# Optimization experiments

Hardware: AMD Instinct MI355X
Metric: run time of the kernel (lower is better)

The kernel has to match this reference:

```python
import jax, jax.numpy as jnp
import numpy as np

K = 512          # codebook size
D = 128          # embedding dim (== num_hiddens, required by the module wiring)
COMMIT = 0.25    # commitment cost
EPS = 1e-10


def conv2d(x, w, b):
    # x: [B,C,H,W], w: [O,I,3,3] (torch OIHW), stride 1, pad 1 -> same spatial size
    y = jax.lax.conv_general_dilated(
        x, w, window_strides=(1, 1), padding=((1, 1), (1, 1)),
        dimension_numbers=("NCHW", "OIHW", "NCHW"))
    return y + b[None, :, None, None]


def conv_transpose2d(x, w, b):
    # torch ConvTranspose2d weight layout is [I, O, kH, kW]; with stride=1, pad=1, k=3
    # it equals a regular conv with the kernel spatially flipped and in/out swapped.
    w2 = jnp.flip(w, axis=(-2, -1)).transpose(1, 0, 2, 3)  # -> OIHW
    return conv2d(x, w2, b)


def setup_inputs() -> dict:
    key = jax.random.key(0)
    ks = jax.random.split(key, 12)
    s = 0.05  # keep activations well-scaled through 8 stacked convs
    return {
        "x":       jax.random.normal(ks[0], (16, 3, 128, 128), jnp.float32),
        "enc_w0":  jax.random.normal(ks[1], (128, 3, 3, 3), jnp.float32) * s,
        "enc_b0":  jax.random.normal(ks[2], (128,), jnp.float32) * s,
        "enc_wh":  jax.random.normal(ks[3], (3, 128, 128, 3, 3), jnp.float32) * s,
        "enc_bh":  jax.random.normal(ks[4], (3, 128), jnp.float32) * s,
        "pre_w":   jax.random.normal(ks[5], (128, 128), jnp.float32) * s,
        "pre_b":   jax.random.normal(ks[6], (128,), jnp.float32) * s,
        "codebook": jax.random.normal(ks[7], (K, D), jnp.float32),  # EMA init: normal_()
        "dec_wh":  jax.random.normal(ks[8], (3, 128, 128, 3, 3), jnp.float32) * s,
        "dec_bh":  jax.random.normal(ks[9], (3, 128), jnp.float32) * s,
        "dec_wl":  jax.random.normal(ks[10], (128, 3, 3, 3), jnp.float32) * s,
        "dec_bl":  jax.random.normal(ks[11], (3,), jnp.float32) * s,
    }


def reference(x, enc_w0, enc_b0, enc_wh, enc_bh, pre_w, pre_b, codebook,
              dec_wh, dec_bh, dec_wl, dec_bl):
    # ---- encoder: stack of 3x3 stride-1 convs (no nonlinearity in the source) ----
    z = conv2d(x, enc_w0, enc_b0)
    for i in range(enc_wh.shape[0]):
        z = conv2d(z, enc_wh[i], enc_bh[i])
    # pre-VQ 1x1 conv
    z = jnp.einsum("bchw,oc->bohw", z, pre_w) + pre_b[None, :, None, None]

    # ---- VectorQuantizerEMA forward (eval mode: EMA buffers not updated) ----
    zt = jnp.transpose(z, (0, 2, 3, 1))          # [B,H,W,D]
    B, H, W, _ = zt.shape
    flat = zt.reshape(-1, D)                      # [N,D]
    d = (jnp.sum(flat * flat, axis=1, keepdims=True)
         + jnp.sum(codebook * codebook, axis=1)
         - 2.0 * flat @ codebook.T)               # [N,K]
    idx = jnp.argmin(d, axis=1)                   # [N]
    quantized = codebook[idx].reshape(B, H, W, D) # gather == one-hot @ codebook

    # commitment loss (EMA variant: only e_latent term)
    e_latent = jnp.mean((jax.lax.stop_gradient(quantized) - zt) ** 2)
    loss = COMMIT * e_latent

    # straight-through estimator
    quantized = zt + jax.lax.stop_gradient(quantized - zt)

    # perplexity from empirical code usage
    counts = jax.ops.segment_sum(jnp.ones_like(idx, jnp.float32), idx, num_segments=K)
    avg_probs = counts / flat.shape[0]
    perplexity = jnp.exp(-jnp.sum(avg_probs * jnp.log(avg_probs + EPS)))

    q = jnp.transpose(quantized, (0, 3, 1, 2))    # back to NCHW

    # ---- decoder: stack of 3x3 stride-1 conv-transposes ----
    h = q
    for i in range(dec_wh.shape[0]):
        h = conv_transpose2d(h, dec_wh[i], dec_bh[i])
    x_recon = conv_transpose2d(h, dec_wl, dec_bl)

    return loss, x_recon, perplexity
```

## Files before the change

### kernel.cpp

```cpp
#include <hip/hip_runtime.h>

namespace {

constexpr int NB = 16, HH = 128, WW = 128, KK = 512, DD = 128;
constexpr int NPIX = NB * HH * WW;
constexpr int NELEM = NPIX * DD;
constexpr int XRECON = NB * 3 * HH * WW;
constexpr int VQ_BLK_PX = 64;
constexpr int VQ_BLOCKS = NPIX / VQ_BLK_PX;

using bf16x8 = __attribute__((ext_vector_type(8))) short;
using f32x4 = __attribute__((ext_vector_type(4))) float;

__device__ __forceinline__ ushort f2bf(float f) {
  unsigned u = __float_as_uint(f);
  return (ushort)((u + 0x7FFFu + ((u >> 16) & 1u)) >> 16);
}

__global__ void zero_counts(int* __restrict__ counts) {
  const int t = threadIdx.x;
  counts[t] = 0;
  counts[t + 256] = 0;
}

__device__ __forceinline__ int swz(int px) { return px + ((px >> 5) << 2); }

__global__ void repack_w(const float* __restrict__ w, float* __restrict__ wr) {
  int i = blockIdx.x * 256 + threadIdx.x;
  int oc = i & 127;
  int tap = (i >> 7) % 9;
  int ci = i / (9 * 128);
  wr[i] = w[(oc * 128 + ci) * 9 + tap];
}

__global__ void repack_wb16(const float* __restrict__ w, ushort* __restrict__ wr) {
  int i = blockIdx.x * 256 + threadIdx.x;
  int j = i & 7;
  int oc = (i >> 3) & 127;
  int cib = (i >> 10) & 15;
  int tap = i >> 14;
  int ci = cib * 8 + j;
  int ky = tap / 3, kx = tap % 3;
  float v = w[((size_t)ci * 128 + oc) * 9 + (2 - ky) * 3 + (2 - kx)];
  wr[i] = f2bf(v);
}

template <int CT>
__global__ __launch_bounds__(256, 5) void conv3x3_s(
    const float* __restrict__ in, const float* __restrict__ wr,
    const float* __restrict__ bias, float* __restrict__ out) {
  __shared__ __align__(16) float s_in[CT][3][148];
  const int tid = threadIdx.x;
  const int b = blockIdx.x >> 7;
  const int y = blockIdx.x & 127;
  const int lane = tid & 63;
  const int wv = __builtin_amdgcn_readfirstlane(tid >> 6);
  const int oc0 = wv << 5;
  const int px0 = lane << 1;

  float acc[32][2];
#pragma unroll
  for (int k = 0; k < 32; ++k) { acc[k][0] = 0.f; acc[k][1] = 0.f; }

  const int f_lo = swz(px0);
  const int f_hi = swz(px0 + 2);

#pragma unroll 1
  for (int ci0 = 0; ci0 < 128; ci0 += CT) {
    for (int i = tid; i < CT * 390; i += 256) {
      int ci = i / 390;
      int rem = i - ci * 390;
      int r = rem / 130;
      int px = rem - r * 130;
      int yy = y + r - 1;
      int xx = px - 1;
      float v = 0.f;
      if (yy >= 0 && yy < HH && xx >= 0 && xx < WW)
        v = in[((b * 128 + ci0 + ci) * HH + yy) * WW + xx];
      s_in[ci][r][swz(px)] = v;
    }
    __syncthreads();
#pragma unroll 1
    for (int ci = 0; ci < CT; ++ci) {
      float ind[3][4];
#pragma unroll
      for (int r = 0; r < 3; ++r) {
        float2 a = *reinterpret_cast<const float2*>(&s_in[ci][r][f_lo]);
        float2 c = *reinterpret_cast<const float2*>(&s_in[ci][r][f_hi]);
        ind[r][0] = a.x; ind[r][1] = a.y; ind[r][2] = c.x; ind[r][3] = c.y;
      }
      const float* wp = wr + (size_t)(ci0 + ci) * 9 * 128 + oc0;
#pragma unroll
      for (int r = 0; r < 3; ++r) {
#pragma unroll
        for (int dx = 0; dx < 3; ++dx) {
          const float* wt = wp + (r * 3 + dx) * 128;
          float ws[32];
#pragma unroll
          for (int k = 0; k < 32; ++k) ws[k] = wt[k];
          float v0 = ind[r][dx], v1 = ind[r][dx + 1];
#pragma unroll
          for (int k = 0; k < 32; ++k) {
            acc[k][0] = __fmaf_rn(ws[k], v0, acc[k][0]);
            acc[k][1] = __fmaf_rn(ws[k], v1, acc[k][1]);
          }
        }
      }
    }
    __syncthreads();
  }
#pragma unroll
  for (int k = 0; k < 32; ++k) {
    int oc = oc0 + k;
    float bv = bias[oc];
    float2 v = {acc[k][0] + bv, acc[k][1] + bv};
    *reinterpret_cast<float2*>(out + ((b * 128 + oc) * HH + y) * WW + px0) = v;
  }
}

__global__ __launch_bounds__(256, 3) void conv_l1(
    const float* __restrict__ in, const float* __restrict__ w,
    const float* __restrict__ bias, float* __restrict__ out) {
  __shared__ __align__(16) double s_in[3][3][74];
  __shared__ __align__(16) float s_w[27][132];
  const int tid = threadIdx.x;
  const int b = blockIdx.x >> 8;
  const int y = (blockIdx.x >> 1) & 127;
  const int x0base = (blockIdx.x & 1) << 6;
  const int ocg = tid >> 3;
  const int pxg = tid & 7;
  const int x0 = pxg * 8;
  const int f0 = pxg * 9;

  double acc[4][8];
#pragma unroll
  for (int k = 0; k < 4; ++k)
#pragma unroll
    for (int p = 0; p < 8; ++p) acc[k][p] = 0.0;

  for (int i = tid; i < 3 * 198; i += 256) {
    int ci = i / 198;
    int rem = i - ci * 198;
    int r = rem / 66;
    int px = rem - r * 66;
    int yy = y + r - 1;
    int xx = x0base + px - 1;
    float v = 0.f;
    if (yy >= 0 && yy < HH && xx >= 0 && xx < WW)
      v = in[((b * 3 + ci) * HH + yy) * WW + xx];
    s_in[ci][r][px + (px >> 3)] = (double)v;
  }
  for (int i = tid; i < 128 * 27; i += 256) {
    int oc = i / 27;
    int j = i - oc * 27;
    s_w[j][oc] = w[oc * 27 + j];
  }
  __syncthreads();
#pragma unroll 1
  for (int ci = 0; ci < 3; ++ci) {
#pragma unroll
    for (int r = 0; r < 3; ++r) {
      double ind[10];
#pragma unroll
      for (int m = 0; m < 8; ++m) ind[m] = s_in[ci][r][f0 + m];
      ind[8] = s_in[ci][r][f0 + 9];
      ind[9] = s_in[ci][r][f0 + 10];
#pragma unroll
      for (int dx = 0; dx < 3; ++dx) {
        float4 w4 = *reinterpret_cast<const float4*>(&s_w[ci * 9 + r * 3 + dx][ocg * 4]);
        double wd[4] = {(double)w4.x, (double)w4.y, (double)w4.z, (double)w4.w};
#pragma unroll
        for (int k = 0; k < 4; ++k)
#pragma unroll
          for (int p = 0; p < 8; ++p) acc[k][p] += wd[k] * ind[p + dx];
      }
    }
  }
#pragma unroll
  for (int k = 0; k < 4; ++k) {
    int oc = ocg * 4 + k;
    double bv = (double)bias[oc];
    float* op = out + ((b * 128 + oc) * HH + y) * WW + x0base + x0;
    float4 v = {(float)(acc[k][0] + bv), (float)(acc[k][1] + bv),
                (float)(acc[k][2] + bv), (float)(acc[k][3] + bv)};
    float4 v2 = {(float)(acc[k][4] + bv), (float)(acc[k][5] + bv),
                 (float)(acc[k][6] + bv), (float)(acc[k][7] + bv)};
    *reinterpret_cast<float4*>(op) = v;
    *reinterpret_cast<float4*>(op + 4) = v2;
  }
}

__global__ __launch_bounds__(256, 3) void prevq_nhwc(
    const float* __restrict__ in, const float* __restrict__ wmat,
    const float* __restrict__ bias, float* __restrict__ flat) {
  __shared__ __align__(16) float s_z[32][68];
  __shared__ __align__(16) float s_w[32][132];
  const int tid = threadIdx.x;
  const int b = blockIdx.x >> 8;
  const int y = (blockIdx.x >> 1) & 127;
  const int x0base = (blockIdx.x & 1) << 6;
  const int ocg = tid >> 3;
  const int pxg = tid & 7;
  float acc[4][8];
#pragma unroll
  for (int k = 0; k < 4; ++k)
#pragma unroll
    for (int p = 0; p < 8; ++p) acc[k][p] = 0.f;

#pragma unroll 1
  for (int c0 = 0; c0 < 128; c0 += 32) {
    for (int t = tid; t < 32 * 64; t += 256) {
      int c = t >> 6, px = t & 63;
      s_z[c][px] = in[((b * 128 + c0 + c) * HH + y) * WW + x0base + px];
    }
    for (int t = tid; t < 32 * 128; t += 256) {
      int o = t >> 5, c = t & 31;
      s_w[c][o] = wmat[o * 128 + c0 + c];
    }
    __syncthreads();
#pragma unroll 1
    for (int c = 0; c < 32; ++c) {
      float f8[8];
#pragma unroll
      for (int p = 0; p < 8; ++p) f8[p] = s_z[c][pxg * 8 + p];
      float4 w4 = *reinterpret_cast<const float4*>(&s_w[c][ocg * 4]);
      float wd[4] = {w4.x, w4.y, w4.z, w4.w};
#pragma unroll
      for (int k = 0; k < 4; ++k)
#pragma unroll
        for (int p = 0; p < 8; ++p) acc[k][p] = __fmaf_rn(wd[k], f8[p], acc[k][p]);
    }
    __syncthreads();
  }
  float bv[4];
#pragma unroll
  for (int k = 0; k < 4; ++k) bv[k] = bias[ocg * 4 + k];
  const int pixbase = (b * HH + y) * WW + x0base + pxg * 8;
#pragma unroll
  for (int p = 0; p < 8; ++p) {
    float* op = flat + (pixbase + p) * DD + ocg * 4;
#pragma unroll
    for (int k = 0; k < 4; ++k) op[k] = __fadd_rn(acc[k][p], bv[k]);
  }
}

__device__ __forceinline__ float pairwise8_sq(const float* v) {
  float r[8];
#pragma unroll
  for (int j = 0; j < 8; ++j) r[j] = __fmul_rn(v[j], v[j]);
#pragma unroll
  for (int i = 8; i < 128; i += 8)
#pragma unroll
    for (int j = 0; j < 8; ++j) r[j] = __fadd_rn(r[j], __fmul_rn(v[i + j], v[i + j]));
  return __fadd_rn(__fadd_rn(__fadd_rn(r[0], r[1]), __fadd_rn(r[2], r[3])),
                   __fadd_rn(__fadd_rn(r[4], r[5]), __fadd_rn(r[6], r[7])));
}

constexpr int SF_OFF = 0;
constexpr int SC_OFF = 33792;
constexpr int SRB_OFF = SC_OFF;
constexpr int SRI_OFF = SC_OFF + 4352;
constexpr int SCN_OFF = SC_OFF + 33792;
constexpr int SZN_OFF = SCN_OFF + 256;
constexpr int SIDX_OFF = SZN_OFF + 256;
constexpr int SRED_OFF = SIDX_OFF + 256;
constexpr int SMEM_BYTES = SRED_OFF + 32;

__global__ __launch_bounds__(256, 2) void vq_fused(
    const float* __restrict__ flat, const float* __restrict__ codebook,
    ushort* __restrict__ q16, float* __restrict__ partial, int* __restrict__ counts) {
  __shared__ __align__(16) char smem[SMEM_BYTES];
  float (*s_f)[132] = reinterpret_cast<float (*)[132]>(smem + SF_OFF);
  float (*s_c)[132] = reinterpret_cast<float (*)[132]>(smem + SC_OFF);
  float (*s_rb)[4][17] = reinterpret_cast<float (*)[4][17]>(smem + SRB_OFF);
  int (*s_ri)[4][17] = reinterpret_cast<int (*)[4][17]>(smem + SRI_OFF);
  float* s_cn = reinterpret_cast<float*>(smem + SCN_OFF);
  float* s_zn = reinterpret_cast<float*>(smem + SZN_OFF);
  int* s_idx = reinterpret_cast<int*>(smem + SIDX_OFF);
  double* s_red = reinterpret_cast<double*>(smem + SRED_OFF);

  const int tid = threadIdx.x;
  const int n0 = blockIdx.x * VQ_BLK_PX;
  const int pxg = tid & 15;
  const int cg = tid >> 4;

  for (int t = tid; t < VQ_BLK_PX * 128; t += 256) {
    int i = t >> 7, d = t & 127;
    s_f[i][d] = flat[(n0 + i) * DD + d];
  }
  __syncthreads();
  if (tid < VQ_BLK_PX) s_zn[tid] = pairwise8_sq(&s_f[tid][0]);

  float best[4] = {3.402823466e+38f, 3.402823466e+38f,
                   3.402823466e+38f, 3.402823466e+38f};
  int bi[4] = {0, 0, 0, 0};

#pragma unroll 1
  for (int c0 = 0; c0 < KK; c0 += 64) {
    for (int t = tid; t < 64 * 128; t += 256) {
      int cc = t >> 7, d = t & 127;
      s_c[cc][d] = codebook[(c0 + cc) * DD + d];
    }
    __syncthreads();
    if (tid < 64) s_cn[tid] = pairwise8_sq(&s_c[tid][0]);
    __syncthreads();
    float acc[4][4];
#pragma unroll
    for (int i = 0; i < 4; ++i)
#pragma unroll
      for (int j = 0; j < 4; ++j) acc[i][j] = 0.f;
#pragma unroll 1
    for (int d0 = 0; d0 < 128; d0 += 4) {
      float4 f4[4], c4[4];
#pragma unroll
      for (int i = 0; i < 4; ++i)
        f4[i] = *reinterpret_cast<const float4*>(&s_f[pxg * 4 + i][d0]);
#pragma unroll
      for (int j = 0; j < 4; ++j)
        c4[j] = *reinterpret_cast<const float4*>(&s_c[cg * 4 + j][d0]);
#pragma unroll
      for (int i = 0; i < 4; ++i) {
#pragma unroll
        for (int j = 0; j < 4; ++j) {
          acc[i][j] = __fmaf_rn(f4[i].x, c4[j].x, acc[i][j]);
          acc[i][j] = __fmaf_rn(f4[i].y, c4[j].y, acc[i][j]);
          acc[i][j] = __fmaf_rn(f4[i].z, c4[j].z, acc[i][j]);
          acc[i][j] = __fmaf_rn(f4[i].w, c4[j].w, acc[i][j]);
        }
      }
    }
#pragma unroll
    for (int i = 0; i < 4; ++i)
#pragma unroll
      for (int j = 0; j < 4; ++j) {
        float score = __fsub_rn(__fadd_rn(s_zn[pxg * 4 + i], s_cn[cg * 4 + j]),
                                __fmul_rn(2.0f, acc[i][j]));
        int code = c0 + cg * 4 + j;
        if (score < best[i]) { best[i] = score; bi[i] = code; }
      }
    __syncthreads();
  }
#pragma unroll
  for (int i = 0; i < 4; ++i) {
    s_rb[pxg][i][cg] = best[i];
    s_ri[pxg][i][cg] = bi[i];
  }
  __syncthreads();
  if (tid < 16) {
    for (int i = 0; i < 4; ++i) {
      float m = s_rb[tid][i][0];
      int mi = s_ri[tid][i][0];
      for (int g = 1; g < 16; ++g) {
        float v = s_rb[tid][i][g];
        int vi = s_ri[tid][i][g];
        if (v < m || (v == m && vi < mi)) { m = v; mi = vi; }
      }
      s_idx[tid * 4 + i] = mi;
    }
  }
  __syncthreads();
  if (tid < VQ_BLK_PX) atomicAdd(&counts[s_idx[tid]], 1);

  const int px = tid & 63;
  const int dg = tid >> 6;
  const int n = n0 + px;
  const int k = s_idx[px];
  const float* crow = codebook + k * DD + dg * 32;
  ushort* qb = q16 + (size_t)n * 128 + dg * 32;
  double s = 0.0;
#pragma unroll 4
  for (int j = 0; j < 32; ++j) {
    float e = crow[j];
    double dd = (double)e - (double)s_f[px][dg * 32 + j];
    s += dd * dd;
    qb[j] = f2bf(e);
  }
  for (int off = 32; off; off >>= 1) s += __shfl_down(s, off);
  if ((tid & 63) == 0) s_red[tid >> 6] = s;
  __syncthreads();
  if (tid == 0)
    partial[blockIdx.x] = (float)(s_red[0] + s_red[1] + s_red[2] + s_red[3]);
}

template <bool LAST>
__global__ __launch_bounds__(256, 4) void dec_mfma(
    const ushort* __restrict__ inq, const ushort* __restrict__ wb,
    const float* __restrict__ bias, float* __restrict__ outf,
    ushort* __restrict__ outq) {
  const int b = blockIdx.x >> 7;
  const int y = blockIdx.x & 127;
  const int lane = threadIdx.x & 63;
  const int wv = threadIdx.x >> 6;
  const int oc0 = wv << 5;
  const int lrow = lane & 15;
  const int lk = lane >> 4;

  f32x4 acc[8][2];
#pragma unroll
  for (int mt = 0; mt < 8; ++mt)
#pragma unroll
    for (int nt = 0; nt < 2; ++nt) acc[mt][nt] = (f32x4){0.f, 0.f, 0.f, 0.f};

#pragma unroll 1
  for (int tap = 0; tap < 9; ++tap) {
    const int ky = tap / 3, kx = tap % 3;
    const int yy = y + ky - 1;
    const bool yok = (yy >= 0) && (yy < HH);
    const ushort* wtap = wb + tap * (16 * 128 * 8);
    const ushort* rowp = inq + ((size_t)(b * HH + yy) * WW) * 128;
#pragma unroll 1
    for (int cb = 0; cb < 4; ++cb) {
      const int cib = cb * 4 + lk;
      bf16x8 bfr0 = *reinterpret_cast<const bf16x8*>(wtap + ((size_t)(cib * 128) + oc0 + lrow) * 8);
      bf16x8 bfr1 = *reinterpret_cast<const bf16x8*>(wtap + ((size_t)(cib * 128) + oc0 + 16 + lrow) * 8);
#pragma unroll
      for (int mt = 0; mt < 8; ++mt) {
        const int xx = mt * 16 + lrow + kx - 1;
        bf16x8 af = {0, 0, 0, 0, 0, 0, 0, 0};
        if (yok && xx >= 0 && xx < WW)
          af = *reinterpret_cast<const bf16x8*>(rowp + (size_t)xx * 128 + cib * 8);
        acc[mt][0] = __builtin_amdgcn_mfma_f32_16x16x32_bf16(af, bfr0, acc[mt][0], 0, 0, 0);
        acc[mt][1] = __builtin_amdgcn_mfma_f32_16x16x32_bf16(af, bfr1, acc[mt][1], 0, 0, 0);
      }
    }
  }
#pragma unroll
  for (int nt = 0; nt < 2; ++nt) {
    const int oc = oc0 + nt * 16 + lrow;
    const float bv = bias[oc];
    if constexpr (LAST) {
#pragma unroll
      for (int mt = 0; mt < 8; ++mt) {
        const int px = mt * 16 + lk * 4;
        float4 v = {acc[mt][nt][0] + bv, acc[mt][nt][1] + bv,
                    acc[mt][nt][2] + bv, acc[mt][nt][3] + bv};
        *reinterpret_cast<float4*>(outf + ((size_t)(b * 128 + oc) * HH + y) * WW + px) = v;
      }
    } else {
#pragma unroll
      for (int mt = 0; mt < 8; ++mt) {
#pragma unroll
        for (int m = 0; m < 4; ++m) {
          const int px = mt * 16 + lk * 4 + m;
          outq[((size_t)(b * HH + y) * WW + px) * 128 + oc] = f2bf(acc[mt][nt][m] + bv);
        }
      }
    }
  }
}

__global__ __launch_bounds__(256, 3) void conv_out3(
    const float* __restrict__ in, const float* __restrict__ w,
    const float* __restrict__ bias, float* __restrict__ out) {
  __shared__ float s_in[16][4][130];
  __shared__ float s_w[128][28];
  const int tid = threadIdx.x;
  const int b = blockIdx.x >> 6;
  const int y0 = (blockIdx.x & 63) << 1;
  const int yloc = tid >> 7;
  const int x = tid & 127;
  const int y = y0 + yloc;
  for (int i = tid; i < 128 * 27; i += 256) {
    int ci = i / 27, rem = i % 27, oc = rem / 9, tap = rem % 9;
    int ky = tap / 3, kx = tap % 3;
    s_w[ci][tap * 3 + oc] = w[((ci * 3 + oc) * 3 + (2 - ky)) * 3 + (2 - kx)];
  }
  float acc[3] = {0.f, 0.f, 0.f};
#pragma unroll 1
  for (int ci0 = 0; ci0 < 128; ci0 += 16) {
    for (int i = tid; i < 16 * 520; i += 256) {
      int ci = i / 520;
      int rem = i - ci * 520;
      int r = rem / 130;
      int px = rem - r * 130;
      int yy = y0 + r - 1;
      float v = 0.f;
      if (yy >= 0 && yy < HH && px >= 1 && px <= 128)
        v = in[((b * 128 + ci0 + ci) * HH + yy) * WW + (px - 1)];
      s_in[ci][r][px] = v;
    }
    __syncthreads();
#pragma unroll 1
    for (int ci = 0; ci < 16; ++ci) {
#pragma unroll
      for (int r = 0; r < 3; ++r) {
        float i3[3] = {s_in[ci][yloc + r][x], s_in[ci][yloc + r][x + 1],
                       s_in[ci][yloc + r][x + 2]};
#pragma unroll
        for (int dx = 0; dx < 3; ++dx)
#pragma unroll
          for (int oc = 0; oc < 3; ++oc)
            acc[oc] += s_w[ci0 + ci][(r * 3 + dx) * 3 + oc] * i3[dx];
      }
    }
    __syncthreads();
  }
#pragma unroll
  for (int oc = 0; oc < 3; ++oc)
    out[((b * 3 + oc) * HH + y) * WW + x] = acc[oc] + bias[oc];
}

__global__ void finalize(const float* __restrict__ partial,
                         const int* __restrict__ counts, float* __restrict__ out) {
  __shared__ double redh[4], reds[4];
  const int tid = threadIdx.x;
  double h = 0.0;
  for (int k = tid; k < KK; k += 256) {
    double p = (double)counts[k] * (1.0 / (double)NPIX);
    h += p * log(p + 1e-10);
  }
  double s = 0.0;
  for (int i = tid; i < VQ_BLOCKS; i += 256) s += (double)partial[i];
  for (int off = 32; off; off >>= 1) {
    h += __shfl_down(h, off);
    s += __shfl_down(s, off);
  }
  if ((tid & 63) == 0) { redh[tid >> 6] = h; reds[tid >> 6] = s; }
  __syncthreads();
  if (tid == 0) {
    double Hs = redh[0] + redh[1] + redh[2] + redh[3];
    double Ss = reds[0] + reds[1] + reds[2] + reds[3];
    out[0] = (float)(0.25 * Ss * (1.0 / (double)NELEM));
    out[1 + XRECON] = (float)exp(-Hs);
  }
}

}

extern "C" void kernel_launch(void* const* d_in, const int* in_sizes, int n_in,
                              void* d_out, int out_size, void* d_ws, size_t ws_size,
                              hipStream_t stream) {
  (void)in_sizes; (void)n_in; (void)out_size; (void)ws_size;
  const float* x       = (const float*)d_in[0];
  const float* enc_w0  = (const float*)d_in[1];
  const float* enc_b0  = (const float*)d_in[2];
  const float* enc_wh  = (const float*)d_in[3];
  const float* enc_bh  = (const float*)d_in[4];
  const float* pre_w   = (const float*)d_in[5];
  const float* pre_b   = (const float*)d_in[6];
  const float* codebook= (const float*)d_in[7];
  const float* dec_wh  = (const float*)d_in[8];
  const float* dec_bh  = (const float*)d_in[9];
  const float* dec_wl  = (const float*)d_in[10];
  const float* dec_bl  = (const float*)d_in[11];
  float* out = (float*)d_out;

  float* A = (float*)d_ws;
  float* Bf = A + NELEM;
  ushort* Q0 = (ushort*)Bf;
  ushort* Q1 = Q0 + NELEM;

  int* counts = (int*)(out + 1);
  float* partial = out + 1 + KK;
  float* wbuf = out + 4612;
  ushort* wb0 = (ushort*)(wbuf + 147456);
  ushort* wb1 = wb0 + 147456;
  ushort* wb2 = wb1 + 147456;

  const int LSTRIDE = 128 * 128 * 9;
  const int RGRID = NB * HH;
  const int CGRID = NB * HH * 2;
  const int WGRID = 576;

  zero_counts<<<1, 256, 0, stream>>>(counts);

  conv_l1<<<CGRID, 256, 0, stream>>>(x, enc_w0, enc_b0, A);
  repack_w<<<WGRID, 256, 0, stream>>>(enc_wh, wbuf);
  conv3x3_s<16><<<RGRID, 256, 0, stream>>>(A, wbuf, enc_bh, Bf);
  repack_w<<<WGRID, 256, 0, stream>>>(enc_wh + LSTRIDE, wbuf);
  conv3x3_s<16><<<RGRID, 256, 0, stream>>>(Bf, wbuf, enc_bh + 128, A);
  repack_w<<<WGRID, 256, 0, stream>>>(enc_wh + 2 * LSTRIDE, wbuf);
  conv3x3_s<16><<<RGRID, 256, 0, stream>>>(A, wbuf, enc_bh + 256, Bf);

  prevq_nhwc<<<CGRID, 256, 0, stream>>>(Bf, pre_w, pre_b, A);

  repack_wb16<<<WGRID, 256, 0, stream>>>(dec_wh, wb0);
  repack_wb16<<<WGRID, 256, 0, stream>>>(dec_wh + LSTRIDE, wb1);
  repack_wb16<<<WGRID, 256, 0, stream>>>(dec_wh + 2 * LSTRIDE, wb2);

  vq_fused<<<VQ_BLOCKS, 256, 0, stream>>>(A, codebook, Q0, partial, counts);

  finalize<<<1, 256, 0, stream>>>(partial, counts, out);

  dec_mfma<false><<<RGRID, 256, 0, stream>>>(Q0, wb0, dec_bh, nullptr, Q1);
  dec_mfma<false><<<RGRID, 256, 0, stream>>>(Q1, wb1, dec_bh + 128, nullptr, Q0);
  dec_mfma<true><<<RGRID, 256, 0, stream>>>(Q0, wb2, dec_bh + 256, A, nullptr);
  conv_out3<<<NB * HH / 2, 256, 0, stream>>>(A, dec_wl, dec_bl, out + 1);
}
```

Baseline: 4.738 ms.

## Retile encoder 3x3 conv to two rows per block with split output channels

```diff
diff --git a/kernel.cpp b/kernel.cpp
--- a/kernel.cpp
+++ b/kernel.cpp
@@ -46,33 +46,36 @@
 }
 
 template <int CT>
-__global__ __launch_bounds__(256, 5) void conv3x3_s(
+__global__ __launch_bounds__(256, 4) void conv3x3_s2(
     const float* __restrict__ in, const float* __restrict__ wr,
     const float* __restrict__ bias, float* __restrict__ out) {
-  __shared__ __align__(16) float s_in[CT][3][148];
+  __shared__ __align__(16) float s_in[CT][4][148];
   const int tid = threadIdx.x;
+  const int ocb = blockIdx.x & 1;
+  const int y0 = ((blockIdx.x >> 1) & 63) << 1;
   const int b = blockIdx.x >> 7;
-  const int y = blockIdx.x & 127;
   const int lane = tid & 63;
   const int wv = __builtin_amdgcn_readfirstlane(tid >> 6);
-  const int oc0 = wv << 5;
+  const int oc0 = ocb * 64 + wv * 16;
   const int px0 = lane << 1;
 
-  float acc[32][2];
-#pragma unroll
-  for (int k = 0; k < 32; ++k) { acc[k][0] = 0.f; acc[k][1] = 0.f; }
+  float acc[16][4];
+#pragma unroll
+  for (int k = 0; k < 16; ++k)
+#pragma unroll
+    for (int p = 0; p < 4; ++p) acc[k][p] = 0.f;
 
   const int f_lo = swz(px0);
   const int f_hi = swz(px0 + 2);
 
 #pragma unroll 1
   for (int ci0 = 0; ci0 < 128; ci0 += CT) {
-    for (int i = tid; i < CT * 390; i += 256) {
-      int ci = i / 390;
-      int rem = i - ci * 390;
+    for (int i = tid; i < CT * 520; i += 256) {
+      int ci = i / 520;
+      int rem = i - ci * 520;
       int r = rem / 130;
       int px = rem - r * 130;
-      int yy = y + r - 1;
+      int yy = y0 + r - 1;
       int xx = px - 1;
       float v = 0.f;
       if (yy >= 0 && yy < HH && xx >= 0 && xx < WW)
@@ -82,9 +85,9 @@
     __syncthreads();
 #pragma unroll 1
     for (int ci = 0; ci < CT; ++ci) {
-      float ind[3][4];
-#pragma unroll
-      for (int r = 0; r < 3; ++r) {
+      float ind[4][4];
+#pragma unroll
+      for (int r = 0; r < 4; ++r) {
         float2 a = *reinterpret_cast<const float2*>(&s_in[ci][r][f_lo]);
         float2 c = *reinterpret_cast<const float2*>(&s_in[ci][r][f_hi]);
         ind[r][0] = a.x; ind[r][1] = a.y; ind[r][2] = c.x; ind[r][3] = c.y;
@@ -95,14 +98,17 @@
 #pragma unroll
         for (int dx = 0; dx < 3; ++dx) {
           const float* wt = wp + (r * 3 + dx) * 128;
-          float ws[32];
-#pragma unroll
-          for (int k = 0; k < 32; ++k) ws[k] = wt[k];
-          float v0 = ind[r][dx], v1 = ind[r][dx + 1];
-#pragma unroll
-          for (int k = 0; k < 32; ++k) {
-            acc[k][0] = __fmaf_rn(ws[k], v0, acc[k][0]);
-            acc[k][1] = __fmaf_rn(ws[k], v1, acc[k][1]);
+          float ws[16];
+#pragma unroll
+          for (int k = 0; k < 16; ++k) ws[k] = wt[k];
+          float a0 = ind[r][dx], a1 = ind[r][dx + 1];
+          float b0 = ind[r + 1][dx], b1 = ind[r + 1][dx + 1];
+#pragma unroll
+          for (int k = 0; k < 16; ++k) {
+            acc[k][0] = __fmaf_rn(ws[k], a0, acc[k][0]);
+            acc[k][1] = __fmaf_rn(ws[k], a1, acc[k][1]);
+            acc[k][2] = __fmaf_rn(ws[k], b0, acc[k][2]);
+            acc[k][3] = __fmaf_rn(ws[k], b1, acc[k][3]);
           }
         }
       }
@@ -110,11 +116,13 @@
     __syncthreads();
   }
 #pragma unroll
-  for (int k = 0; k < 32; ++k) {
+  for (int k = 0; k < 16; ++k) {
     int oc = oc0 + k;
     float bv = bias[oc];
-    float2 v = {acc[k][0] + bv, acc[k][1] + bv};
-    *reinterpret_cast<float2*>(out + ((b * 128 + oc) * HH + y) * WW + px0) = v;
+    float2 v0 = {acc[k][0] + bv, acc[k][1] + bv};
+    float2 v1 = {acc[k][2] + bv, acc[k][3] + bv};
+    *reinterpret_cast<float2*>(out + ((b * 128 + oc) * HH + y0) * WW + px0) = v0;
+    *reinterpret_cast<float2*>(out + ((b * 128 + oc) * HH + y0 + 1) * WW + px0) = v1;
   }
 }
 
@@ -566,11 +574,11 @@
 
   conv_l1<<<CGRID, 256, 0, stream>>>(x, enc_w0, enc_b0, A);
   repack_w<<<WGRID, 256, 0, stream>>>(enc_wh, wbuf);
-  conv3x3_s<16><<<RGRID, 256, 0, stream>>>(A, wbuf, enc_bh, Bf);
+  conv3x3_s2<16><<<RGRID, 256, 0, stream>>>(A, wbuf, enc_bh, Bf);
   repack_w<<<WGRID, 256, 0, stream>>>(enc_wh + LSTRIDE, wbuf);
-  conv3x3_s<16><<<RGRID, 256, 0, stream>>>(Bf, wbuf, enc_bh + 128, A);
+  conv3x3_s2<16><<<RGRID, 256, 0, stream>>>(Bf, wbuf, enc_bh + 128, A);
   repack_w<<<WGRID, 256, 0, stream>>>(enc_wh + 2 * LSTRIDE, wbuf);
-  conv3x3_s<16><<<RGRID, 256, 0, stream>>>(A, wbuf, enc_bh + 256, Bf);
+  conv3x3_s2<16><<<RGRID, 256, 0, stream>>>(A, wbuf, enc_bh + 256, Bf);
 
   prevq_nhwc<<<CGRID, 256, 0, stream>>>(Bf, pre_w, pre_b, A);
 
```

Measured after the change: 4.703 ms. No clear change (-0.7%).
